# Kernel optimization log

Hardware: AMD Instinct MI355X
Metric: run time of the kernel (lower is better)

Reference implementation:

```python
import jax, jax.numpy as jnp
import numpy as np

B, T, D = 8, 4096, 1024

def setup_inputs() -> dict:
    key = jax.random.key(0)
    ks = jax.random.split(key, 7)
    s1 = 1.0 / np.sqrt(D)
    return {
        "x":  jax.random.normal(ks[0], (B, T, D), dtype=jnp.float32),
        "W1": jax.random.normal(ks[1], (D, D), dtype=jnp.float32) * s1,   # attn_1.weight [out,in]
        "b1": jnp.zeros((D,), dtype=jnp.float32),
        "w2": jax.random.normal(ks[2], (1, D), dtype=jnp.float32) * s1,   # attn_2.weight [1,in]
        "b2": jnp.zeros((1,), dtype=jnp.float32),
        "Wc": jax.random.normal(ks[3], (D, 2 * D), dtype=jnp.float32) * (1.0 / np.sqrt(2 * D)),
        "bc": jnp.zeros((D,), dtype=jnp.float32),
    }

def reference(x, W1, b1, w2, b2, Wc, bc):
    # additive attention scores: [B, T, 1] -> [B, T]
    h = jnp.tanh(jnp.einsum('btd,ed->bte', x, W1) + b1)
    s = (jnp.einsum('btd,od->bto', h, w2) + b2)[..., 0]          # [B, T]
    # causal prefix softmax via cumulative sums (single O(T) pass).
    # softmax is shift-invariant, so subtracting the global per-batch max is stable.
    m = jnp.max(s, axis=1, keepdims=True)                        # [B, 1]
    e = jnp.exp(s - m)                                           # [B, T]
    num = jnp.cumsum(e[..., None] * x, axis=1)                   # [B, T, D]
    den = jnp.cumsum(e, axis=1)[..., None]                       # [B, T, 1]
    ctx = num / den                                              # [B, T, D]
    combined = jnp.concatenate((ctx, x), axis=2)                 # [B, T, 2D]
    out = jnp.tanh(jnp.einsum('btk,dk->btd', combined, Wc) + bc)
    return out
```

## Files before the change

kernel.cpp:

```cpp
#include <hip/hip_runtime.h>
#include <cmath>


#define Mtot 32768
#define Dd 1024
#define Tt 4096
#define Bb 8
#define NCHUNK 64
#define TCH 64

typedef __bf16 bf16x8 __attribute__((ext_vector_type(8)));
typedef float f32x4 __attribute__((ext_vector_type(4)));

__device__ __forceinline__ unsigned short f2bf(float f) {
  unsigned int u = __float_as_uint(f);
  unsigned int r = (u + 0x7FFFu + ((u >> 16) & 1u)) >> 16;
  return (unsigned short)r;
}
__device__ __forceinline__ float bf2f(unsigned short s) {
  return __uint_as_float(((unsigned int)s) << 16);
}
__device__ __forceinline__ float tanh_fast(float x) {
  return 1.0f - __fdividef(2.0f, __expf(2.0f * x) + 1.0f);
}

__device__ __forceinline__ void gload16(const unsigned short* g, unsigned short* l) {
  __builtin_amdgcn_global_load_lds(
      (const __attribute__((address_space(1))) unsigned int*)g,
      (__attribute__((address_space(3))) unsigned int*)l, 16, 0, 0);
}

__device__ __forceinline__ void mfma_core(
    const unsigned short* __restrict__ A0, const unsigned short* __restrict__ A1,
    const unsigned short* __restrict__ W, int ldw, int Ktot,
    int m0, int n0, unsigned short* As, unsigned short* Bs, f32x4 acc[4][4]) {
  int tid = threadIdx.x;
  int lane = tid & 63, w = tid >> 6;
  int wm = w >> 1, wn = w & 1;
  int quad = lane >> 4, c = lane & 15;
  int lrow = lane >> 3;
  int col8 = (lane & 7) ^ lrow;

  for (int k0 = 0; k0 < Ktot; k0 += 64) {
    const unsigned short* Asrc = (k0 < 1024) ? A0 : A1;
    int ka = k0 & 1023;
#pragma unroll
    for (int j = 0; j < 4; ++j) {
      int row = w * 32 + j * 8 + lrow;
      gload16(Asrc + (size_t)(m0 + row) * 1024 + ka + col8 * 8, As + w * 2048 + j * 512);
      gload16(W + (size_t)(n0 + row) * ldw + k0 + col8 * 8, Bs + w * 2048 + j * 512);
    }
    __syncthreads();
#pragma unroll
    for (int ks = 0; ks < 2; ++ks) {
      bf16x8 af[4], bfr[4];
#pragma unroll
      for (int i = 0; i < 4; ++i) {
        int ra = wm * 64 + i * 16 + c;
        int pa = (ks * 4 + quad) ^ (ra & 7);
        af[i] = *(const bf16x8*)(As + ra * 64 + pa * 8);
        int rb = wn * 64 + i * 16 + c;
        int pb = (ks * 4 + quad) ^ (rb & 7);
        bfr[i] = *(const bf16x8*)(Bs + rb * 64 + pb * 8);
      }
#pragma unroll
      for (int i = 0; i < 4; ++i)
#pragma unroll
        for (int jn = 0; jn < 4; ++jn)
          acc[i][jn] = __builtin_amdgcn_mfma_f32_16x16x32_bf16(af[i], bfr[jn], acc[i][jn], 0, 0, 0);
    }
    __syncthreads();
  }
}

__global__ __launch_bounds__(256) void gemm_s(
    const unsigned short* __restrict__ xb, const unsigned short* __restrict__ W1b,
    const float* __restrict__ b1, const float* __restrict__ w2, float* __restrict__ s) {
  __shared__ unsigned short As[128 * 64];
  __shared__ unsigned short Bs[128 * 64];
  f32x4 acc[4][4];
#pragma unroll
  for (int i = 0; i < 4; ++i)
#pragma unroll
    for (int j = 0; j < 4; ++j) acc[i][j] = (f32x4){0.f, 0.f, 0.f, 0.f};
  int m0 = blockIdx.x * 128, n0 = blockIdx.y * 128;
  mfma_core(xb, xb, W1b, 1024, 1024, m0, n0, As, Bs, acc);
  int tid = threadIdx.x, lane = tid & 63, w = tid >> 6;
  int wm = w >> 1, wn = w & 1, quad = lane >> 4, c = lane & 15;
#pragma unroll
  for (int i = 0; i < 4; ++i) {
#pragma unroll
    for (int r = 0; r < 4; ++r) {
      float p = 0.f;
#pragma unroll
      for (int jn = 0; jn < 4; ++jn) {
        int n = n0 + wn * 64 + jn * 16 + c;
        p += w2[n] * tanh_fast(acc[i][jn][r] + b1[n]);
      }
      p += __shfl_xor(p, 1, 64);
      p += __shfl_xor(p, 2, 64);
      p += __shfl_xor(p, 4, 64);
      p += __shfl_xor(p, 8, 64);
      if (c == 0) atomicAdd(&s[m0 + wm * 64 + i * 16 + quad * 4 + r], p);
    }
  }
}

__global__ __launch_bounds__(256) void gemm_out(
    const unsigned short* __restrict__ qb, const unsigned short* __restrict__ xb,
    const unsigned short* __restrict__ Wcb, const float* __restrict__ bc_,
    float* __restrict__ out) {
  __shared__ unsigned short As[128 * 64];
  __shared__ unsigned short Bs[128 * 64];
  f32x4 acc[4][4];
#pragma unroll
  for (int i = 0; i < 4; ++i)
#pragma unroll
    for (int j = 0; j < 4; ++j) acc[i][j] = (f32x4){0.f, 0.f, 0.f, 0.f};
  int m0 = blockIdx.x * 128, n0 = blockIdx.y * 128;
  mfma_core(qb, xb, Wcb, 2048, 2048, m0, n0, As, Bs, acc);
  int tid = threadIdx.x, lane = tid & 63, w = tid >> 6;
  int wm = w >> 1, wn = w & 1, quad = lane >> 4, c = lane & 15;
#pragma unroll
  for (int i = 0; i < 4; ++i)
#pragma unroll
    for (int jn = 0; jn < 4; ++jn) {
      int n = n0 + wn * 64 + jn * 16 + c;
      float bias = bc_[n];
#pragma unroll
      for (int r = 0; r < 4; ++r) {
        int m = m0 + wm * 64 + i * 16 + quad * 4 + r;
        out[(size_t)m * Dd + n] = tanh_fast(acc[i][jn][r] + bias);
      }
    }
}

__global__ __launch_bounds__(256) void cast_all(
    const float4* __restrict__ x, const float4* __restrict__ W1,
    const float4* __restrict__ Wc, ushort4* __restrict__ xb,
    ushort4* __restrict__ W1b, ushort4* __restrict__ Wcb,
    float4* __restrict__ s) {
  int i = blockIdx.x * 256 + threadIdx.x;
  if (i < 8388608) {
    float4 v = x[i];
    ushort4 o;
    o.x = f2bf(v.x); o.y = f2bf(v.y); o.z = f2bf(v.z); o.w = f2bf(v.w);
    xb[i] = o;
  } else if (i < 8650752) {
    int p = i - 8388608;
    float4 v = W1[p];
    ushort4 o;
    o.x = f2bf(v.x); o.y = f2bf(v.y); o.z = f2bf(v.z); o.w = f2bf(v.w);
    W1b[p] = o;
  } else if (i < 9175040) {
    int p = i - 8650752;
    float4 v = Wc[p];
    ushort4 o;
    o.x = f2bf(v.x); o.y = f2bf(v.y); o.z = f2bf(v.z); o.w = f2bf(v.w);
    Wcb[p] = o;
  } else {
    s[i - 9175040] = (float4){0.f, 0.f, 0.f, 0.f};
  }
}

__global__ __launch_bounds__(256) void softmax_scan(
    const float* __restrict__ s, float* __restrict__ e, float* __restrict__ den) {
  int b = blockIdx.x, tid = threadIdx.x;
  int lane = tid & 63, wid = tid >> 6;
  __shared__ float redm[4], wsum[4];
  const float4* sb4 = (const float4*)(s + (size_t)b * Tt);
  float v[16];
#pragma unroll
  for (int j = 0; j < 4; ++j) {
    float4 f = sb4[tid * 4 + j];
    v[j * 4 + 0] = f.x; v[j * 4 + 1] = f.y; v[j * 4 + 2] = f.z; v[j * 4 + 3] = f.w;
  }
  float m = v[0];
#pragma unroll
  for (int j = 1; j < 16; ++j) m = fmaxf(m, v[j]);
#pragma unroll
  for (int off = 32; off > 0; off >>= 1) m = fmaxf(m, __shfl_xor(m, off, 64));
  if (lane == 0) redm[wid] = m;
  __syncthreads();
  m = fmaxf(fmaxf(redm[0], redm[1]), fmaxf(redm[2], redm[3]));
  float ev[16];
  float ls = 0.f;
#pragma unroll
  for (int j = 0; j < 16; ++j) { ev[j] = __expf(v[j] - m); ls += ev[j]; }
  float sc = ls;
#pragma unroll
  for (int off = 1; off < 64; off <<= 1) {
    float tt = __shfl_up(sc, off, 64);
    if (lane >= off) sc += tt;
  }
  if (lane == 63) wsum[wid] = sc;
  __syncthreads();
  float woff = 0.f;
#pragma unroll
  for (int w = 0; w < 4; ++w) woff += (w < wid) ? wsum[w] : 0.f;
  float run = sc - ls + woff;
  float4* eb4 = (float4*)(e + (size_t)b * Tt);
  float4* db4 = (float4*)(den + (size_t)b * Tt);
#pragma unroll
  for (int j = 0; j < 4; ++j) {
    float4 eo, doo;
    run += ev[j * 4 + 0]; eo.x = ev[j * 4 + 0]; doo.x = run;
    run += ev[j * 4 + 1]; eo.y = ev[j * 4 + 1]; doo.y = run;
    run += ev[j * 4 + 2]; eo.z = ev[j * 4 + 2]; doo.z = run;
    run += ev[j * 4 + 3]; eo.w = ev[j * 4 + 3]; doo.w = run;
    eb4[tid * 4 + j] = eo;
    db4[tid * 4 + j] = doo;
  }
}

__global__ __launch_bounds__(1024) void chunk_sums(
    const unsigned short* __restrict__ xb, const float* __restrict__ e,
    float* __restrict__ S) {
  int bc = blockIdx.x;
  int b = bc >> 6, c = bc & 63;
  int d = threadIdx.x;
  const unsigned short* xp = xb + ((size_t)(b * Tt + c * TCH)) * Dd + d;
  const float* eb = e + (size_t)b * Tt + c * TCH;
  float acc = 0.f;
#pragma unroll 8
  for (int t = 0; t < TCH; ++t) acc += eb[t] * bf2f(xp[(size_t)t * Dd]);
  S[((size_t)bc) * Dd + d] = acc;
}

__global__ __launch_bounds__(256) void chunk_prefix(float* __restrict__ S) {
  int idx = blockIdx.x * 256 + threadIdx.x;
  int b = idx >> 10, d = idx & 1023;
  float* Sb = S + (size_t)b * NCHUNK * Dd + d;
  float acc = 0.f;
#pragma unroll 8
  for (int c = 0; c < NCHUNK; ++c) {
    float t = Sb[(size_t)c * Dd];
    Sb[(size_t)c * Dd] = acc;
    acc += t;
  }
}

__global__ __launch_bounds__(1024) void scan_q(
    const unsigned short* __restrict__ xb, const float* __restrict__ e,
    const float* __restrict__ den, const float* __restrict__ S,
    unsigned short* __restrict__ qb) {
  int bc = blockIdx.x;
  int b = bc >> 6, c = bc & 63;
  int d = threadIdx.x;
  int tbase = b * Tt + c * TCH;
  float acc = S[((size_t)bc) * Dd + d];
  const unsigned short* xp = xb + (size_t)tbase * Dd + d;
  const float* eb = e + tbase;
  const float* db = den + tbase;
  unsigned short* qp = qb + (size_t)tbase * Dd + d;
#pragma unroll 4
  for (int t = 0; t < TCH; ++t) {
    acc += eb[t] * bf2f(xp[(size_t)t * Dd]);
    qp[(size_t)t * Dd] = f2bf(acc * __fdividef(1.0f, db[t]));
  }
}

extern "C" void kernel_launch(void* const* d_in, const int* in_sizes, int n_in,
                              void* d_out, int out_size, void* d_ws, size_t ws_size,
                              hipStream_t stream) {
  const float* x  = (const float*)d_in[0];
  const float* W1 = (const float*)d_in[1];
  const float* b1 = (const float*)d_in[2];
  const float* w2 = (const float*)d_in[3];
  const float* Wc = (const float*)d_in[5];
  const float* bc = (const float*)d_in[6];
  float* out = (float*)d_out;

  float* ws = (float*)d_ws;
  float* s_buf   = ws;
  float* e_buf   = ws + 32768;
  float* den_buf = ws + 65536;
  float* S_buf   = ws + 98304;
  unsigned short* qb  = (unsigned short*)(ws + 622592);
  unsigned short* xb  = (unsigned short*)(ws + 17399808);
  unsigned short* W1b = (unsigned short*)(ws + 34177024);
  unsigned short* Wcb = (unsigned short*)(ws + 34701312);

  cast_all<<<35872, 256, 0, stream>>>((const float4*)x, (const float4*)W1,
                                      (const float4*)Wc, (ushort4*)xb,
                                      (ushort4*)W1b, (ushort4*)Wcb,
                                      (float4*)s_buf);

  gemm_s<<<dim3(Mtot / 128, Dd / 128), 256, 0, stream>>>(xb, W1b, b1, w2, s_buf);
  softmax_scan<<<Bb, 256, 0, stream>>>(s_buf, e_buf, den_buf);
  chunk_sums<<<Bb * NCHUNK, 1024, 0, stream>>>(xb, e_buf, S_buf);
  chunk_prefix<<<Bb * Dd / 256, 256, 0, stream>>>(S_buf);
  scan_q<<<Bb * NCHUNK, 1024, 0, stream>>>(xb, e_buf, den_buf, S_buf, qb);
  gemm_out<<<dim3(Mtot / 128, Dd / 128), 256, 0, stream>>>(qb, xb, Wcb, bc, out);
}
```

Baseline: 536.3 us.

## Use 256x256 double-buffered MFMA GEMM tiles with block swizzle

Both GEMMs move from a 128x128 tile with 4 waves to a 256x256 tile with 8 waves. Global-to-LDS loads are double-buffered so the next K-tile prefetches while MFMAs run on the current one, and s_setprio raises priority around the MFMA bursts. A block-index swizzle groups nearby tiles for L2 reuse, and the gemm_s epilogue hoists the w2/b1 loads. The cost is 128KB of LDS per block, which may limit occupancy to one block per CU despite launch_bounds(512,2), plus higher register pressure from 8x4 accumulators.

```diff
diff --git a/kernel.cpp b/kernel.cpp
--- a/kernel.cpp
+++ b/kernel.cpp
@@ -30,109 +30,155 @@
       (__attribute__((address_space(3))) unsigned int*)l, 16, 0, 0);
 }
 
-__device__ __forceinline__ void mfma_core(
+__device__ __forceinline__ void mfma_core256(
     const unsigned short* __restrict__ A0, const unsigned short* __restrict__ A1,
     const unsigned short* __restrict__ W, int ldw, int Ktot,
-    int m0, int n0, unsigned short* As, unsigned short* Bs, f32x4 acc[4][4]) {
-  int tid = threadIdx.x;
-  int lane = tid & 63, w = tid >> 6;
-  int wm = w >> 1, wn = w & 1;
-  int quad = lane >> 4, c = lane & 15;
-  int lrow = lane >> 3;
-  int col8 = (lane & 7) ^ lrow;
-
-  for (int k0 = 0; k0 < Ktot; k0 += 64) {
-    const unsigned short* Asrc = (k0 < 1024) ? A0 : A1;
-    int ka = k0 & 1023;
-#pragma unroll
-    for (int j = 0; j < 4; ++j) {
-      int row = w * 32 + j * 8 + lrow;
-      gload16(Asrc + (size_t)(m0 + row) * 1024 + ka + col8 * 8, As + w * 2048 + j * 512);
-      gload16(W + (size_t)(n0 + row) * ldw + k0 + col8 * 8, Bs + w * 2048 + j * 512);
+    int m0, int n0, unsigned short* lds, f32x4 acc[8][4]) {
+  const int tid = threadIdx.x;
+  const int lane = tid & 63, w = tid >> 6;
+  const int wm = w >> 2, wn = w & 3;
+  const int quad = lane >> 4, c = lane & 15;
+  const int lrow = lane >> 3;
+  const int col8 = (lane & 7) ^ lrow;
+  const int NK = Ktot >> 6;
+
+#define STG(dst, kt_) do {                                                        \
+    int k0_ = (kt_) << 6;                                                         \
+    const unsigned short* Asrc_ = (k0_ < 1024) ? A0 : A1;                         \
+    int ka_ = k0_ & 1023;                                                         \
+    _Pragma("unroll")                                                             \
+    for (int j = 0; j < 4; ++j) {                                                 \
+      int rb_ = j * 64 + w * 8;                                                   \
+      gload16(Asrc_ + (size_t)(m0 + rb_ + lrow) * 1024 + ka_ + col8 * 8,          \
+              (dst) + rb_ * 64);                                                  \
+      gload16(W + (size_t)(n0 + rb_ + lrow) * ldw + k0_ + col8 * 8,               \
+              (dst) + 16384 + rb_ * 64);                                          \
+    }                                                                             \
+  } while (0)
+
+  STG(lds, 0);
+
+#pragma unroll 1
+  for (int kt = 0; kt < NK; ++kt) {
+    unsigned short* cur = lds + (kt & 1) * 32768;
+    unsigned short* nxt = lds + ((kt + 1) & 1) * 32768;
+    if (kt + 1 < NK) {
+      STG(nxt, kt + 1);
+      asm volatile("s_waitcnt vmcnt(8)" ::: "memory");
+    } else {
+      asm volatile("s_waitcnt vmcnt(0)" ::: "memory");
     }
-    __syncthreads();
-#pragma unroll
-    for (int ks = 0; ks < 2; ++ks) {
-      bf16x8 af[4], bfr[4];
-#pragma unroll
-      for (int i = 0; i < 4; ++i) {
-        int ra = wm * 64 + i * 16 + c;
+    __builtin_amdgcn_s_barrier();
+    asm volatile("" ::: "memory");
+
+    const unsigned short* As = cur;
+    const unsigned short* Bs = cur + 16384;
+    bf16x8 bfr[4];
+#pragma unroll
+    for (int p = 0; p < 4; ++p) {
+      const int ks = p >> 1, mh = p & 1;
+      if (mh == 0) {
+#pragma unroll
+        for (int jn = 0; jn < 4; ++jn) {
+          int rb = wn * 64 + jn * 16 + c;
+          int pb = (ks * 4 + quad) ^ (rb & 7);
+          bfr[jn] = *(const bf16x8*)(Bs + rb * 64 + pb * 8);
+        }
+      }
+      bf16x8 af[4];
+#pragma unroll
+      for (int ii = 0; ii < 4; ++ii) {
+        int ra = wm * 128 + (mh * 4 + ii) * 16 + c;
         int pa = (ks * 4 + quad) ^ (ra & 7);
-        af[i] = *(const bf16x8*)(As + ra * 64 + pa * 8);
-        int rb = wn * 64 + i * 16 + c;
-        int pb = (ks * 4 + quad) ^ (rb & 7);
-        bfr[i] = *(const bf16x8*)(Bs + rb * 64 + pb * 8);
+        af[ii] = *(const bf16x8*)(As + ra * 64 + pa * 8);
       }
-#pragma unroll
-      for (int i = 0; i < 4; ++i)
+      asm volatile("" ::: "memory");
+      __builtin_amdgcn_s_barrier();
+      asm volatile("s_waitcnt lgkmcnt(0)" ::: "memory");
+      __builtin_amdgcn_sched_barrier(0);
+      __builtin_amdgcn_s_setprio(1);
+#pragma unroll
+      for (int ii = 0; ii < 4; ++ii)
 #pragma unroll
         for (int jn = 0; jn < 4; ++jn)
-          acc[i][jn] = __builtin_amdgcn_mfma_f32_16x16x32_bf16(af[i], bfr[jn], acc[i][jn], 0, 0, 0);
+          acc[mh * 4 + ii][jn] = __builtin_amdgcn_mfma_f32_16x16x32_bf16(
+              af[ii], bfr[jn], acc[mh * 4 + ii][jn], 0, 0, 0);
+      __builtin_amdgcn_s_setprio(0);
+      asm volatile("" ::: "memory");
+      __builtin_amdgcn_s_barrier();
+      asm volatile("" ::: "memory");
     }
-    __syncthreads();
-  }
-}
-
-__global__ __launch_bounds__(256) void gemm_s(
+  }
+#undef STG
+}
+
+__global__ __launch_bounds__(512, 2) void gemm_s(
     const unsigned short* __restrict__ xb, const unsigned short* __restrict__ W1b,
     const float* __restrict__ b1, const float* __restrict__ w2, float* __restrict__ s) {
-  __shared__ unsigned short As[128 * 64];
-  __shared__ unsigned short Bs[128 * 64];
-  f32x4 acc[4][4];
-#pragma unroll
-  for (int i = 0; i < 4; ++i)
+  __shared__ __align__(16) unsigned short lds[65536];
+  f32x4 acc[8][4];
+#pragma unroll
+  for (int i = 0; i < 8; ++i)
 #pragma unroll
     for (int j = 0; j < 4; ++j) acc[i][j] = (f32x4){0.f, 0.f, 0.f, 0.f};
-  int m0 = blockIdx.x * 128, n0 = blockIdx.y * 128;
-  mfma_core(xb, xb, W1b, 1024, 1024, m0, n0, As, Bs, acc);
+  int bid = blockIdx.x;
+  int swz = (bid & 7) * 64 + (bid >> 3);
+  int m0 = (swz >> 2) * 256, n0 = (swz & 3) * 256;
+  mfma_core256(xb, xb, W1b, 1024, 1024, m0, n0, lds, acc);
   int tid = threadIdx.x, lane = tid & 63, w = tid >> 6;
-  int wm = w >> 1, wn = w & 1, quad = lane >> 4, c = lane & 15;
-#pragma unroll
-  for (int i = 0; i < 4; ++i) {
+  int wm = w >> 2, wn = w & 3, quad = lane >> 4, c = lane & 15;
+  float w2v[4], b1v[4];
+#pragma unroll
+  for (int jn = 0; jn < 4; ++jn) {
+    int n = n0 + wn * 64 + jn * 16 + c;
+    w2v[jn] = w2[n];
+    b1v[jn] = b1[n];
+  }
+#pragma unroll
+  for (int i = 0; i < 8; ++i) {
 #pragma unroll
     for (int r = 0; r < 4; ++r) {
       float p = 0.f;
 #pragma unroll
-      for (int jn = 0; jn < 4; ++jn) {
-        int n = n0 + wn * 64 + jn * 16 + c;
-        p += w2[n] * tanh_fast(acc[i][jn][r] + b1[n]);
-      }
+      for (int jn = 0; jn < 4; ++jn) p += w2v[jn] * tanh_fast(acc[i][jn][r] + b1v[jn]);
       p += __shfl_xor(p, 1, 64);
       p += __shfl_xor(p, 2, 64);
       p += __shfl_xor(p, 4, 64);
       p += __shfl_xor(p, 8, 64);
-      if (c == 0) atomicAdd(&s[m0 + wm * 64 + i * 16 + quad * 4 + r], p);
+      if (c == 0) atomicAdd(&s[m0 + wm * 128 + i * 16 + quad * 4 + r], p);
     }
   }
 }
 
-__global__ __launch_bounds__(256) void gemm_out(
+__global__ __launch_bounds__(512, 2) void gemm_out(
     const unsigned short* __restrict__ qb, const unsigned short* __restrict__ xb,
     const unsigned short* __restrict__ Wcb, const float* __restrict__ bc_,
     float* __restrict__ out) {
-  __shared__ unsigned short As[128 * 64];
-  __shared__ unsigned short Bs[128 * 64];
-  f32x4 acc[4][4];
-#pragma unroll
-  for (int i = 0; i < 4; ++i)
+  __shared__ __align__(16) unsigned short lds[65536];
+  f32x4 acc[8][4];
+#pragma unroll
+  for (int i = 0; i < 8; ++i)
 #pragma unroll
     for (int j = 0; j < 4; ++j) acc[i][j] = (f32x4){0.f, 0.f, 0.f, 0.f};
-  int m0 = blockIdx.x * 128, n0 = blockIdx.y * 128;
-  mfma_core(qb, xb, Wcb, 2048, 2048, m0, n0, As, Bs, acc);
+  int bid = blockIdx.x;
+  int swz = (bid & 7) * 64 + (bid >> 3);
+  int m0 = (swz >> 2) * 256, n0 = (swz & 3) * 256;
+  mfma_core256(qb, xb, Wcb, 2048, 2048, m0, n0, lds, acc);
   int tid = threadIdx.x, lane = tid & 63, w = tid >> 6;
-  int wm = w >> 1, wn = w & 1, quad = lane >> 4, c = lane & 15;
-#pragma unroll
-  for (int i = 0; i < 4; ++i)
-#pragma unroll
-    for (int jn = 0; jn < 4; ++jn) {
-      int n = n0 + wn * 64 + jn * 16 + c;
-      float bias = bc_[n];
+  int wm = w >> 2, wn = w & 3, quad = lane >> 4, c = lane & 15;
+#pragma unroll
+  for (int jn = 0; jn < 4; ++jn) {
+    int n = n0 + wn * 64 + jn * 16 + c;
+    float bias = bc_[n];
+#pragma unroll
+    for (int i = 0; i < 8; ++i) {
 #pragma unroll
       for (int r = 0; r < 4; ++r) {
-        int m = m0 + wm * 64 + i * 16 + quad * 4 + r;
+        int m = m0 + wm * 128 + i * 16 + quad * 4 + r;
         out[(size_t)m * Dd + n] = tanh_fast(acc[i][jn][r] + bias);
       }
     }
+  }
 }
 
 __global__ __launch_bounds__(256) void cast_all(
@@ -286,10 +332,10 @@
                                       (ushort4*)W1b, (ushort4*)Wcb,
                                       (float4*)s_buf);
 
-  gemm_s<<<dim3(Mtot / 128, Dd / 128), 256, 0, stream>>>(xb, W1b, b1, w2, s_buf);
+  gemm_s<<<512, 512, 0, stream>>>(xb, W1b, b1, w2, s_buf);
   softmax_scan<<<Bb, 256, 0, stream>>>(s_buf, e_buf, den_buf);
   chunk_sums<<<Bb * NCHUNK, 1024, 0, stream>>>(xb, e_buf, S_buf);
   chunk_prefix<<<Bb * Dd / 256, 256, 0, stream>>>(S_buf);
   scan_q<<<Bb * NCHUNK, 1024, 0, stream>>>(xb, e_buf, den_buf, S_buf, qb);
-  gemm_out<<<dim3(Mtot / 128, Dd / 128), 256, 0, stream>>>(qb, xb, Wcb, bc, out);
-}
+  gemm_out<<<512, 512, 0, stream>>>(qb, xb, Wcb, bc, out);
+}
```

After: 496.3 us. 1.08x faster.
